# Performance work log

Hardware: AMD Instinct MI355X
Metric: run time of the kernel (lower is better)

## Reference

```python
import jax, jax.numpy as jnp
import numpy as np

N = 20000; DEG = 32; E = N * DEG; F = 142; D = 32; H = 4; HD = H * D; C = 2
_BN = np.float32(1.0 / np.sqrt(1.0 + 1e-5))  # eval-mode BatchNorm1d with running mean 0 / var 1


def _prelu(x, a):
    return jnp.where(x >= 0, x, a * x)


def _layernorm(x, g, b):
    m = x.mean(-1, keepdims=True)
    v = x.var(-1, keepdims=True)
    return (x - m) / jnp.sqrt(v + 1e-5) * g + b


def _conv(h, src, dst, Wq, bq, Wk, bk, Wv, bv, Ws, bs, Wg, bg, lng, lnb, a):
    # TransformerConv: u_dot_v attention (q from src, k from dst), edge softmax over
    # incoming edges of each dst node, u_mul_e + sum aggregation, gated skip, LN, PReLU.
    n = h.shape[0]
    q = (h @ Wq + bq).reshape(n, H, D)
    k = (h @ Wk + bk).reshape(n, H, D)
    v = (h @ Wv + bv).reshape(n, H, D)
    scores = jnp.einsum('ehd,ehd->eh', q[src], k[dst]) / np.float32(np.sqrt(D))  # [E,H]
    m = jax.ops.segment_max(scores, dst, num_segments=n)
    p = jnp.exp(scores - m[dst])
    s = jax.ops.segment_sum(p, dst, num_segments=n)
    sa = p / s[dst]                                                              # [E,H]
    agg = jax.ops.segment_sum(v[src] * sa[..., None], dst, num_segments=n)       # [N,H,D]
    agg = agg.reshape(n, HD)
    skip = h @ Ws + bs
    g = jax.nn.sigmoid(jnp.concatenate([skip, agg, skip - agg], -1) @ Wg + bg)
    rst = g * skip + (1.0 - g) * agg
    return _prelu(_layernorm(rst, lng, lnb), a)


def setup_inputs() -> dict:
    ks = jax.random.split(jax.random.key(0), 64)
    def nrm(i, shape, s=0.05):
        return (jax.random.normal(ks[i], shape) * s).astype(jnp.float32)
    inp = {}
    inp['features'] = jax.random.normal(ks[0], (N, F), jnp.float32)
    inp['label_emb'] = nrm(1, (C + 1, F)).at[C].set(0.0)  # padding_idx = n_classes
    inp['W1'] = nrm(2, (F, HD)); inp['b1'] = jnp.zeros(HD)
    inp['W2'] = nrm(3, (F, HD)); inp['b2'] = jnp.zeros(HD)
    inp['bn0_g'] = jnp.ones(HD); inp['bn0_b'] = jnp.zeros(HD)
    inp['a3'] = 0.25 * jnp.ones(1)
    inp['W3'] = nrm(4, (HD, F)); inp['b3'] = jnp.zeros(F)
    i = 5
    for l, fin in enumerate([F, HD]):
        inp[f'Wq{l}'] = nrm(i, (fin, HD)); i += 1
        inp[f'bq{l}'] = jnp.zeros(HD)
        inp[f'Wk{l}'] = nrm(i, (fin, HD)); i += 1
        inp[f'bk{l}'] = jnp.zeros(HD)
        inp[f'Wv{l}'] = nrm(i, (fin, HD)); i += 1
        inp[f'bv{l}'] = jnp.zeros(HD)
        inp[f'Ws{l}'] = nrm(i, (fin, HD)); i += 1
        inp[f'bs{l}'] = jnp.zeros(HD)
        inp[f'Wg{l}'] = nrm(i, (3 * HD, 1)); i += 1
        inp[f'bg{l}'] = jnp.zeros(1)
        inp[f'ln{l}_g'] = jnp.ones(HD)
        inp[f'ln{l}_b'] = jnp.zeros(HD)
    inp['a_conv'] = 0.25 * jnp.ones(1)  # single PReLU instance shared by both conv layers
    inp['W4'] = nrm(i, (HD, HD)); i += 1; inp['b4'] = jnp.zeros(HD)
    inp['bn1_g'] = jnp.ones(HD); inp['bn1_b'] = jnp.zeros(HD)
    inp['a5'] = 0.25 * jnp.ones(1)
    inp['W5'] = nrm(i, (HD, C)); i += 1; inp['b5'] = jnp.zeros(C)
    inp['labels'] = jax.random.randint(ks[40], (N,), 0, C + 1)
    inp['edge_src'] = jax.random.randint(ks[41], (E,), 0, N)
    inp['edge_dst'] = jnp.repeat(jnp.arange(N), DEG)  # every node has in-degree DEG
    return inp


def reference(features, label_emb, W1, b1, W2, b2, bn0_g, bn0_b, a3, W3, b3,
              Wq0, bq0, Wk0, bk0, Wv0, bv0, Ws0, bs0, Wg0, bg0, ln0_g, ln0_b,
              Wq1, bq1, Wk1, bk1, Wv1, bv1, Ws1, bs1, Wg1, bg1, ln1_g, ln1_b,
              a_conv, W4, b4, bn1_g, bn1_b, a5, W5, b5,
              labels, edge_src, edge_dst):
    le = label_emb[labels]                                   # [N,F]
    le = features @ W1 + b1 + le @ W2 + b2                   # [N,HD]
    le = _prelu(le * _BN * bn0_g + bn0_b, a3) @ W3 + b3      # BN -> PReLU -> Linear
    h = features + le
    h = _conv(h, edge_src, edge_dst, Wq0, bq0, Wk0, bk0, Wv0, bv0, Ws0, bs0, Wg0, bg0, ln0_g, ln0_b, a_conv)
    h = _conv(h, edge_src, edge_dst, Wq1, bq1, Wk1, bk1, Wv1, bv1, Ws1, bs1, Wg1, bg1, ln1_g, ln1_b, a_conv)
    x = h @ W4 + b4
    x = _prelu(x * _BN * bn1_g + bn1_b, a5)
    return x @ W5 + b5                                       # [N, n_classes]
```

## Files before the change

kernel.cpp:

```cpp
#include <hip/hip_runtime.h>
#include <math.h>

#define N_NODES 20000
#define DEG 32
#define F_IN 142
#define HD 128
#define NHEAD 4
#define DHEAD 32
#define N_CLS 2

#define BN_SCALE 0.9999950000374997f
#define INV_SQRT_D 0.17677669529663687f

typedef short v8s __attribute__((ext_vector_type(8)));
typedef float v4f __attribute__((ext_vector_type(4)));

__device__ __forceinline__ unsigned short f2bf(float f) {
    unsigned u = __float_as_uint(f);
    return (unsigned short)((u + 0x7fffu + ((u >> 16) & 1u)) >> 16);
}
__device__ __forceinline__ unsigned pack2bf(float a, float b) {
    return (unsigned)f2bf(a) | ((unsigned)f2bf(b) << 16);
}
__device__ __forceinline__ float bf2f(unsigned short s) {
    return __uint_as_float((unsigned)s << 16);
}
__device__ __forceinline__ float bflo(unsigned u) { return __uint_as_float(u << 16); }
__device__ __forceinline__ float bfhi(unsigned u) { return __uint_as_float(u & 0xffff0000u); }

__device__ __forceinline__ v8s pack8(float4 f0, float4 f1) {
    union { v8s s; unsigned u[4]; } x;
    x.u[0] = pack2bf(f0.x, f0.y);
    x.u[1] = pack2bf(f0.z, f0.w);
    x.u[2] = pack2bf(f1.x, f1.y);
    x.u[3] = pack2bf(f1.z, f1.w);
    return x.s;
}

__global__ void kE0(const float* __restrict__ lemb, const float* __restrict__ W2,
                    const float* __restrict__ b1, const float* __restrict__ b2,
                    float* __restrict__ E) {
    __shared__ float sl[F_IN];
    int l = blockIdx.x, c = threadIdx.x;
    for (int f = c; f < F_IN; f += HD) sl[f] = lemb[l * F_IN + f];
    __syncthreads();
    float acc = b1[c] + b2[c];
    for (int f = 0; f < F_IN; ++f) acc += sl[f] * W2[f * HD + c];
    E[l * HD + c] = acc;
}

template<int KC, int K>
__global__ void kSwiz4(const float* Wa, const float* Wb, const float* Wc,
                       const float* Wd, short* __restrict__ out) {
    const float* Wt[4] = {Wa, Wb, Wc, Wd};
    const float* W = Wt[blockIdx.y];
    const int tile = blockIdx.x;
    const int kc = tile % KC, nt = tile / KC;
    const int L = threadIdx.x;
    const int n = nt * 16 + (L & 15);
    const int kb = kc * 32 + (L >> 4) * 8;
    short v[8] __attribute__((aligned(16)));
    #pragma unroll
    for (int j = 0; j < 8; ++j) {
        int k = kb + j;
        v[j] = (k < K) ? (short)f2bf(W[(size_t)k * HD + n]) : (short)0;
    }
    short* dst = out + (size_t)blockIdx.y * (8 * KC * 64 * 8) + ((size_t)tile * 64 + L) * 8;
    *(uint4*)dst = *(const uint4*)v;
}

template<int KC, int K>
__global__ void kSwiz1(const float* __restrict__ W, short* __restrict__ out) {
    const int tile = blockIdx.x;
    const int kc = tile % KC, nt = tile / KC;
    const int L = threadIdx.x;
    const int n = nt * 16 + (L & 15);
    const int kb = kc * 32 + (L >> 4) * 8;
    short v[8] __attribute__((aligned(16)));
    #pragma unroll
    for (int j = 0; j < 8; ++j) {
        int k = kb + j;
        v[j] = (k < K) ? (short)f2bf(W[(size_t)k * HD + n]) : (short)0;
    }
    *(uint4*)(out + ((size_t)tile * 64 + L) * 8) = *(const uint4*)v;
}

__global__ void kSwizW3(const float* __restrict__ W3, short* __restrict__ out) {
    const int tile = blockIdx.x;
    const int kc = tile & 3, nt = tile >> 2;
    const int L = threadIdx.x;
    const int n = nt * 16 + (L & 15);
    const int kb = kc * 32 + (L >> 4) * 8;
    short v[8] __attribute__((aligned(16)));
    #pragma unroll
    for (int j = 0; j < 8; ++j)
        v[j] = (n < F_IN) ? (short)f2bf(W3[(size_t)(kb + j) * F_IN + n]) : (short)0;
    *(uint4*)(out + ((size_t)tile * 64 + L) * 8) = *(const uint4*)v;
}

__global__ __launch_bounds__(256) void kAB_m(const float* __restrict__ feat,
        const short* __restrict__ W1f, const short* __restrict__ W3f,
        const int* __restrict__ labels, const float* __restrict__ E,
        const float* __restrict__ bng, const float* __restrict__ bnb,
        const float* __restrict__ a3, const float* __restrict__ b3,
        float* __restrict__ h) {
    __shared__ float4 sAv[32 * 164 / 4];
    __shared__ uint4  sTv[32 * 136 / 8];
    __shared__ int sLab[32];
    float* sA = (float*)sAv;
    unsigned short* sT = (unsigned short*)sTv;
    const int tid = threadIdx.x;
    const int row0 = blockIdx.x * 32;
    for (int idx = tid; idx < 32 * F_IN; idx += 256) {
        int r = idx / F_IN, c = idx - r * F_IN;
        sA[r * 164 + c] = feat[(size_t)(row0 + r) * F_IN + c];
    }
    {   const int ZC = 160 - F_IN;
        for (int idx = tid; idx < 32 * ZC; idx += 256) {
            int r = idx / ZC, c = idx - r * ZC;
            sA[r * 164 + F_IN + c] = 0.f;
        }
    }
    if (tid < 32) sLab[tid] = labels[row0 + tid];
    __syncthreads();

    const int lane = tid & 63, w = tid >> 6;
    const int m = lane & 15, q = lane >> 4;
    const int nt0 = w * 2, nt1 = nt0 + 1;

    v4f acc00 = {0.f,0.f,0.f,0.f}, acc01 = acc00, acc10 = acc00, acc11 = acc00;
    #pragma unroll
    for (int kc = 0; kc < 5; ++kc) {
        const float* r0 = sA + m * 164 + kc * 32 + q * 8;
        const float* r1 = sA + (16 + m) * 164 + kc * 32 + q * 8;
        v8s a0 = pack8(*(const float4*)r0, *(const float4*)(r0 + 4));
        v8s a1 = pack8(*(const float4*)r1, *(const float4*)(r1 + 4));
        v8s b0 = *(const v8s*)(W1f + ((size_t)((nt0 * 5 + kc) * 64 + lane)) * 8);
        v8s b1 = *(const v8s*)(W1f + ((size_t)((nt1 * 5 + kc) * 64 + lane)) * 8);
        acc00 = __builtin_amdgcn_mfma_f32_16x16x32_bf16(a0, b0, acc00, 0, 0, 0);
        acc01 = __builtin_amdgcn_mfma_f32_16x16x32_bf16(a0, b1, acc01, 0, 0, 0);
        acc10 = __builtin_amdgcn_mfma_f32_16x16x32_bf16(a1, b0, acc10, 0, 0, 0);
        acc11 = __builtin_amdgcn_mfma_f32_16x16x32_bf16(a1, b1, acc11, 0, 0, 0);
    }
    const int c0 = w * 32 + m, c1 = c0 + 16;
    {
        const float g0 = bng[c0] * BN_SCALE, g1 = bng[c1] * BN_SCALE;
        const float bb0 = bnb[c0], bb1 = bnb[c1];
        const float al = a3[0];
        #pragma unroll
        for (int rt = 0; rt < 2; ++rt) {
            v4f A0 = rt ? acc10 : acc00;
            v4f A1 = rt ? acc11 : acc01;
            #pragma unroll
            for (int i = 0; i < 4; ++i) {
                const int r = rt * 16 + q * 4 + i;
                const int lab = sLab[r];
                float y0 = (A0[i] + E[lab * HD + c0]) * g0 + bb0;
                float y1 = (A1[i] + E[lab * HD + c1]) * g1 + bb1;
                y0 = (y0 >= 0.f) ? y0 : al * y0;
                y1 = (y1 >= 0.f) ? y1 : al * y1;
                sT[r * 136 + c0] = f2bf(y0);
                sT[r * 136 + c1] = f2bf(y1);
            }
        }
    }
    __syncthreads();

    v4f d00 = {0.f,0.f,0.f,0.f}, d01 = d00, d10 = d00, d11 = d00, e0 = d00, e1 = d00;
    #pragma unroll
    for (int kc = 0; kc < 4; ++kc) {
        v8s a0 = *(const v8s*)(sT + m * 136 + kc * 32 + q * 8);
        v8s a1 = *(const v8s*)(sT + (16 + m) * 136 + kc * 32 + q * 8);
        v8s b0 = *(const v8s*)(W3f + ((size_t)((nt0 * 4 + kc) * 64 + lane)) * 8);
        v8s b1 = *(const v8s*)(W3f + ((size_t)((nt1 * 4 + kc) * 64 + lane)) * 8);
        d00 = __builtin_amdgcn_mfma_f32_16x16x32_bf16(a0, b0, d00, 0, 0, 0);
        d01 = __builtin_amdgcn_mfma_f32_16x16x32_bf16(a0, b1, d01, 0, 0, 0);
        d10 = __builtin_amdgcn_mfma_f32_16x16x32_bf16(a1, b0, d10, 0, 0, 0);
        d11 = __builtin_amdgcn_mfma_f32_16x16x32_bf16(a1, b1, d11, 0, 0, 0);
        if (w == 3) {
            v8s b2 = *(const v8s*)(W3f + ((size_t)((8 * 4 + kc) * 64 + lane)) * 8);
            e0 = __builtin_amdgcn_mfma_f32_16x16x32_bf16(a0, b2, e0, 0, 0, 0);
            e1 = __builtin_amdgcn_mfma_f32_16x16x32_bf16(a1, b2, e1, 0, 0, 0);
        }
    }
    const float b30 = b3[c0], b31 = b3[c1];
    #pragma unroll
    for (int rt = 0; rt < 2; ++rt) {
        v4f D0 = rt ? d10 : d00;
        v4f D1 = rt ? d11 : d01;
        #pragma unroll
        for (int i = 0; i < 4; ++i) {
            const int r = row0 + rt * 16 + q * 4 + i;
            h[(size_t)r * F_IN + c0] = feat[(size_t)r * F_IN + c0] + D0[i] + b30;
            h[(size_t)r * F_IN + c1] = feat[(size_t)r * F_IN + c1] + D1[i] + b31;
        }
    }
    if (w == 3) {
        const int c2 = 128 + m;
        if (c2 < F_IN) {
            const float b32 = b3[c2];
            #pragma unroll
            for (int i = 0; i < 4; ++i) {
                const int ra = row0 + q * 4 + i;
                const int rb = ra + 16;
                h[(size_t)ra * F_IN + c2] = feat[(size_t)ra * F_IN + c2] + e0[i] + b32;
                h[(size_t)rb * F_IN + c2] = feat[(size_t)rb * F_IN + c2] + e1[i] + b32;
            }
        }
    }
}

template<int K, int LDSK, int KC>
__global__ __launch_bounds__(256) void kC4_mf(const float* __restrict__ A,
        const short* __restrict__ WfBase,
        const float* __restrict__ bq, const float* __restrict__ bk,
        const float* __restrict__ bv, const float* __restrict__ bs,
        unsigned short* __restrict__ qh, unsigned short* __restrict__ kh,
        unsigned short* __restrict__ vh, float* __restrict__ sOut) {
    __shared__ float4 sAv[32 * LDSK / 4];
    float* sA = (float*)sAv;
    const int tid = threadIdx.x;
    const int row0 = blockIdx.x * 32;
    for (int idx = tid; idx < 32 * K; idx += 256) {
        int r = idx / K, c = idx - r * K;
        sA[r * LDSK + c] = A[(size_t)(row0 + r) * K + c];
    }
    if (K < KC * 32) {
        const int ZC = KC * 32 - K;
        for (int idx = tid; idx < 32 * ZC; idx += 256) {
            int r = idx / ZC, c = idx - r * ZC;
            sA[r * LDSK + K + c] = 0.f;
        }
    }
    __syncthreads();

    const int lane = tid & 63, w = tid >> 6;
    const int m = lane & 15, q = lane >> 4;
    const int nt0 = w * 2, nt1 = nt0 + 1;

    v8s afr0[KC], afr1[KC];
    #pragma unroll
    for (int kc = 0; kc < KC; ++kc) {
        const float* r0 = sA + m * LDSK + kc * 32 + q * 8;
        const float* r1 = sA + (16 + m) * LDSK + kc * 32 + q * 8;
        afr0[kc] = pack8(*(const float4*)r0, *(const float4*)(r0 + 4));
        afr1[kc] = pack8(*(const float4*)r1, *(const float4*)(r1 + 4));
    }

    const int c0 = w * 32 + m, c1 = c0 + 16;
    #pragma unroll
    for (int mat = 0; mat < 4; ++mat) {
        const short* Wf = WfBase + (size_t)mat * (KC * 4096);
        const float* bias = (mat == 0) ? bq : (mat == 1) ? bk : (mat == 2) ? bv : bs;
        v4f acc00 = {0.f,0.f,0.f,0.f}, acc01 = acc00, acc10 = acc00, acc11 = acc00;
        #pragma unroll
        for (int kc = 0; kc < KC; ++kc) {
            v8s b0 = *(const v8s*)(Wf + ((size_t)((nt0 * KC + kc) * 64 + lane)) * 8);
            v8s b1 = *(const v8s*)(Wf + ((size_t)((nt1 * KC + kc) * 64 + lane)) * 8);
            acc00 = __builtin_amdgcn_mfma_f32_16x16x32_bf16(afr0[kc], b0, acc00, 0, 0, 0);
            acc01 = __builtin_amdgcn_mfma_f32_16x16x32_bf16(afr0[kc], b1, acc01, 0, 0, 0);
            acc10 = __builtin_amdgcn_mfma_f32_16x16x32_bf16(afr1[kc], b0, acc10, 0, 0, 0);
            acc11 = __builtin_amdgcn_mfma_f32_16x16x32_bf16(afr1[kc], b1, acc11, 0, 0, 0);
        }
        const float b0v = bias[c0], b1v = bias[c1];
        if (mat < 3) {
            unsigned short* outh = (mat == 0) ? qh : (mat == 1) ? kh : vh;
            unsigned short* outw = outh + ((size_t)w * N_NODES + row0) * DHEAD;
            #pragma unroll
            for (int rt = 0; rt < 2; ++rt) {
                v4f A0 = rt ? acc10 : acc00;
                v4f A1 = rt ? acc11 : acc01;
                #pragma unroll
                for (int i = 0; i < 4; ++i) {
                    const int r = rt * 16 + q * 4 + i;
                    outw[(size_t)r * DHEAD + m]      = f2bf(A0[i] + b0v);
                    outw[(size_t)r * DHEAD + 16 + m] = f2bf(A1[i] + b1v);
                }
            }
        } else {
            #pragma unroll
            for (int rt = 0; rt < 2; ++rt) {
                v4f A0 = rt ? acc10 : acc00;
                v4f A1 = rt ? acc11 : acc01;
                #pragma unroll
                for (int i = 0; i < 4; ++i) {
                    const int r = rt * 16 + q * 4 + i;
                    sOut[(size_t)(row0 + r) * HD + c0] = A0[i] + b0v;
                    sOut[(size_t)(row0 + r) * HD + c1] = A1[i] + b1v;
                }
            }
        }
    }
}

__global__ __launch_bounds__(256) void kD_h(const unsigned short* __restrict__ qh,
        const unsigned short* __restrict__ kh, const unsigned short* __restrict__ vh,
        const int* __restrict__ esrc, float* __restrict__ agg) {
    __shared__ float sk[8][DHEAD];
    __shared__ int ssrc[8][DEG];
    __shared__ float sa[8][DEG];
    const int h = blockIdx.y;
    const int n0 = blockIdx.x * 8;
    const int t = threadIdx.x;
    const int j = t >> 5, e = t & 31;

    ssrc[j][e] = esrc[n0 * DEG + t];
    if (t < 128) {
        unsigned u = *((const unsigned*)(kh + ((size_t)h * N_NODES + n0) * DHEAD) + t);
        float* skf = &sk[0][0];
        skf[2 * t]     = bflo(u);
        skf[2 * t + 1] = bfhi(u);
    }
    __syncthreads();

    const int src = ssrc[j][e];
    const uint4* qp = (const uint4*)(qh + ((size_t)h * N_NODES + src) * DHEAD);
    const float* kj = sk[j];
    float sc = 0.f;
    #pragma unroll
    for (int i = 0; i < 4; ++i) {
        uint4 u = qp[i];
        sc = fmaf(bflo(u.x), kj[i * 8 + 0], sc);
        sc = fmaf(bfhi(u.x), kj[i * 8 + 1], sc);
        sc = fmaf(bflo(u.y), kj[i * 8 + 2], sc);
        sc = fmaf(bfhi(u.y), kj[i * 8 + 3], sc);
        sc = fmaf(bflo(u.z), kj[i * 8 + 4], sc);
        sc = fmaf(bfhi(u.z), kj[i * 8 + 5], sc);
        sc = fmaf(bflo(u.w), kj[i * 8 + 6], sc);
        sc = fmaf(bfhi(u.w), kj[i * 8 + 7], sc);
    }
    sc *= INV_SQRT_D;
    float m = sc;
    #pragma unroll
    for (int off = 16; off > 0; off >>= 1)
        m = fmaxf(m, __shfl_xor(m, off, 32));
    float p = expf(sc - m);
    float ssum = p;
    #pragma unroll
    for (int off = 16; off > 0; off >>= 1)
        ssum += __shfl_xor(ssum, off, 32);
    sa[j][e] = p / ssum;
    __syncthreads();

    const int d = t & 31;
    const unsigned short* vbase = vh + (size_t)h * N_NODES * DHEAD + d;
    float acc = 0.f;
    #pragma unroll
    for (int e2 = 0; e2 < DEG; ++e2) {
        const int s2 = ssrc[j][e2];
        acc = fmaf(bf2f(vbase[(size_t)s2 * DHEAD]), sa[j][e2], acc);
    }
    agg[(size_t)(n0 + j) * HD + h * DHEAD + d] = acc;
}

__device__ __forceinline__ float blockSum128(float v, float* s2, int tid) {
    #pragma unroll
    for (int o = 32; o > 0; o >>= 1) v += __shfl_xor(v, o, 64);
    if ((tid & 63) == 0) s2[tid >> 6] = v;
    __syncthreads();
    float r = s2[0] + s2[1];
    __syncthreads();
    return r;
}

__global__ void kE(const float* __restrict__ skip, const float* __restrict__ agg,
                   const float* __restrict__ Wg, const float* __restrict__ bg,
                   const float* __restrict__ lng, const float* __restrict__ lnb,
                   const float* __restrict__ ac,
                   float* __restrict__ hout) {
    __shared__ float red[2];
    int n = blockIdx.x, c = threadIdx.x;
    float sk = skip[n * HD + c], ag = agg[n * HD + c];
    float part = sk * Wg[c] + ag * Wg[HD + c] + (sk - ag) * Wg[2 * HD + c];
    float z = blockSum128(part, red, c) + bg[0];
    float g = 1.f / (1.f + expf(-z));
    float r = g * sk + (1.f - g) * ag;
    float mean = blockSum128(r, red, c) * (1.f / HD);
    float dv = r - mean;
    float var = blockSum128(dv * dv, red, c) * (1.f / HD);
    float y = dv * rsqrtf(var + 1e-5f) * lng[c] + lnb[c];
    float a = ac[0];
    hout[n * HD + c] = (y >= 0.f) ? y : a * y;
}

__global__ __launch_bounds__(256) void kF_mf2(const float* __restrict__ A,
        const short* __restrict__ W4f, const float* __restrict__ b4,
        const float* __restrict__ bng, const float* __restrict__ bnb,
        const float* __restrict__ a5, const float* __restrict__ W5,
        const float* __restrict__ b5, float* __restrict__ out) {
    __shared__ float4 sAv[32 * 132 / 4];
    float* sA = (float*)sAv;
    const int tid = threadIdx.x;
    const int row0 = blockIdx.x * 32;
    for (int idx = tid; idx < 32 * HD; idx += 256) {
        int r = idx >> 7, c = idx & 127;
        sA[r * 132 + c] = A[(size_t)(row0 + r) * HD + c];
    }
    __syncthreads();
    const int lane = tid & 63, w = tid >> 6;
    const int m = lane & 15, q = lane >> 4;
    const int nt0 = w * 2, nt1 = nt0 + 1;
    v4f acc00 = {0.f,0.f,0.f,0.f}, acc01 = acc00, acc10 = acc00, acc11 = acc00;
    #pragma unroll
    for (int kc = 0; kc < 4; ++kc) {
        const float* r0 = sA + m * 132 + kc * 32 + q * 8;
        const float* r1 = sA + (16 + m) * 132 + kc * 32 + q * 8;
        v8s a0 = pack8(*(const float4*)r0, *(const float4*)(r0 + 4));
        v8s a1 = pack8(*(const float4*)r1, *(const float4*)(r1 + 4));
        v8s b0 = *(const v8s*)(W4f + ((size_t)((nt0 * 4 + kc) * 64 + lane)) * 8);
        v8s b1 = *(const v8s*)(W4f + ((size_t)((nt1 * 4 + kc) * 64 + lane)) * 8);
        acc00 = __builtin_amdgcn_mfma_f32_16x16x32_bf16(a0, b0, acc00, 0, 0, 0);
        acc01 = __builtin_amdgcn_mfma_f32_16x16x32_bf16(a0, b1, acc01, 0, 0, 0);
        acc10 = __builtin_amdgcn_mfma_f32_16x16x32_bf16(a1, b0, acc10, 0, 0, 0);
        acc11 = __builtin_amdgcn_mfma_f32_16x16x32_bf16(a1, b1, acc11, 0, 0, 0);
    }
    __syncthreads();
    const int c0 = w * 32 + m, c1 = c0 + 16;
    const float g0 = bng[c0] * BN_SCALE, g1 = bng[c1] * BN_SCALE;
    const float bb0 = bnb[c0], bb1 = bnb[c1];
    const float b40 = b4[c0], b41 = b4[c1];
    const float al = a5[0];
    #pragma unroll
    for (int rt = 0; rt < 2; ++rt) {
        v4f A0 = rt ? acc10 : acc00;
        v4f A1 = rt ? acc11 : acc01;
        #pragma unroll
        for (int i = 0; i < 4; ++i) {
            const int r = rt * 16 + q * 4 + i;
            float y0 = (A0[i] + b40) * g0 + bb0;
            float y1 = (A1[i] + b41) * g1 + bb1;
            y0 = (y0 >= 0.f) ? y0 : al * y0;
            y1 = (y1 >= 0.f) ? y1 : al * y1;
            sA[r * 132 + c0] = y0;
            sA[r * 132 + c1] = y1;
        }
    }
    __syncthreads();
    if (tid < 64) {
        const int r = tid >> 1, cls = tid & 1;
        const float* yr = sA + r * 132;
        float s = b5[cls];
        #pragma unroll 8
        for (int c = 0; c < HD; ++c)
            s = fmaf(yr[c], W5[c * 2 + cls], s);
        out[(size_t)(row0 + r) * N_CLS + cls] = s;
    }
}

extern "C" void kernel_launch(void* const* d_in, const int* in_sizes, int n_in,
                              void* d_out, int out_size, void* d_ws, size_t ws_size,
                              hipStream_t stream) {
    const float* feat  = (const float*)d_in[0];
    const float* lemb  = (const float*)d_in[1];
    const float* W1    = (const float*)d_in[2];
    const float* b1    = (const float*)d_in[3];
    const float* W2    = (const float*)d_in[4];
    const float* b2    = (const float*)d_in[5];
    const float* bn0g  = (const float*)d_in[6];
    const float* bn0b  = (const float*)d_in[7];
    const float* a3    = (const float*)d_in[8];
    const float* W3    = (const float*)d_in[9];
    const float* b3    = (const float*)d_in[10];
    const float* aconv = (const float*)d_in[35];
    const float* W4    = (const float*)d_in[36];
    const float* b4    = (const float*)d_in[37];
    const float* bn1g  = (const float*)d_in[38];
    const float* bn1b  = (const float*)d_in[39];
    const float* a5    = (const float*)d_in[40];
    const float* W5    = (const float*)d_in[41];
    const float* b5    = (const float*)d_in[42];
    const int*   labels = (const int*)d_in[43];
    const int*   esrc   = (const int*)d_in[44];

    char* ws = (char*)d_ws;
    float* bh  = (float*)ws;                       ws += sizeof(float) * N_NODES * F_IN;
    float* bs  = (float*)ws;                       ws += sizeof(float) * N_NODES * HD;
    float* bag = (float*)ws;                       ws += sizeof(float) * N_NODES * HD;
    float* bh2 = (float*)ws;                       ws += sizeof(float) * N_NODES * HD;
    unsigned short* bqh = (unsigned short*)ws;     ws += sizeof(short) * N_NODES * HD;
    unsigned short* bkh = (unsigned short*)ws;     ws += sizeof(short) * N_NODES * HD;
    unsigned short* bvh = (unsigned short*)ws;     ws += sizeof(short) * N_NODES * HD;
    short* Wf0 = (short*)ws;                       ws += sizeof(short) * 4 * 20480;
    short* Wf1 = (short*)ws;                       ws += sizeof(short) * 4 * 16384;
    short* W1f = (short*)ws;                       ws += sizeof(short) * 20480;
    short* W3f = (short*)ws;                       ws += sizeof(short) * 36 * 512;
    short* W4f = (short*)ws;                       ws += sizeof(short) * 16384;
    float* bE = bag;
    float* out = (float*)d_out;

    dim3 gT(N_NODES / 32);
    dim3 gD(N_NODES / 8, NHEAD);

    kE0<<<dim3(3), HD, 0, stream>>>(lemb, W2, b1, b2, bE);
    kSwiz4<5, F_IN><<<dim3(40, 4), 64, 0, stream>>>(
        (const float*)d_in[11], (const float*)d_in[13],
        (const float*)d_in[15], (const float*)d_in[17], Wf0);
    kSwiz4<4, HD><<<dim3(32, 4), 64, 0, stream>>>(
        (const float*)d_in[23], (const float*)d_in[25],
        (const float*)d_in[27], (const float*)d_in[29], Wf1);
    kSwiz1<5, F_IN><<<dim3(40), 64, 0, stream>>>(W1, W1f);
    kSwizW3<<<dim3(36), 64, 0, stream>>>(W3, W3f);
    kSwiz1<4, HD><<<dim3(32), 64, 0, stream>>>(W4, W4f);

    kAB_m<<<gT, 256, 0, stream>>>(feat, W1f, W3f, labels, bE, bn0g, bn0b, a3, b3, bh);

    kC4_mf<F_IN, 164, 5><<<gT, 256, 0, stream>>>(bh, Wf0,
        (const float*)d_in[12], (const float*)d_in[14],
        (const float*)d_in[16], (const float*)d_in[18],
        bqh, bkh, bvh, bs);
    kD_h<<<gD, 256, 0, stream>>>(bqh, bkh, bvh, esrc, bag);
    kE<<<dim3(N_NODES), HD, 0, stream>>>(bs, bag, (const float*)d_in[19], (const float*)d_in[20],
        (const float*)d_in[21], (const float*)d_in[22], aconv, bh2);

    kC4_mf<HD, 132, 4><<<gT, 256, 0, stream>>>(bh2, Wf1,
        (const float*)d_in[24], (const float*)d_in[26],
        (const float*)d_in[28], (const float*)d_in[30],
        bqh, bkh, bvh, bs);
    kD_h<<<gD, 256, 0, stream>>>(bqh, bkh, bvh, esrc, bag);
    kE<<<dim3(N_NODES), HD, 0, stream>>>(bs, bag, (const float*)d_in[31], (const float*)d_in[32],
        (const float*)d_in[33], (const float*)d_in[34], aconv, bh2);

    kF_mf2<<<gT, 256, 0, stream>>>(bh2, W4f, b4, bn1g, bn1b, a5, W5, b5, out);
}
```

Measured before the change: 328.5 us.

## Fuse attention aggregation with gated skip, LayerNorm and PReLU per node block

```diff
diff --git a/kernel.cpp b/kernel.cpp
--- a/kernel.cpp
+++ b/kernel.cpp
@@ -50,9 +50,9 @@
 }
 
 template<int KC, int K>
-__global__ void kSwiz4(const float* Wa, const float* Wb, const float* Wc,
-                       const float* Wd, short* __restrict__ out) {
-    const float* Wt[4] = {Wa, Wb, Wc, Wd};
+__global__ void kSwiz5(const float* Wa, const float* Wb, const float* Wc,
+                       const float* Wd, const float* We, short* __restrict__ out) {
+    const float* Wt[5] = {Wa, Wb, Wc, Wd, We};
     const float* W = Wt[blockIdx.y];
     const int tile = blockIdx.x;
     const int kc = tile % KC, nt = tile / KC;
@@ -67,22 +67,6 @@
     }
     short* dst = out + (size_t)blockIdx.y * (8 * KC * 64 * 8) + ((size_t)tile * 64 + L) * 8;
     *(uint4*)dst = *(const uint4*)v;
-}
-
-template<int KC, int K>
-__global__ void kSwiz1(const float* __restrict__ W, short* __restrict__ out) {
-    const int tile = blockIdx.x;
-    const int kc = tile % KC, nt = tile / KC;
-    const int L = threadIdx.x;
-    const int n = nt * 16 + (L & 15);
-    const int kb = kc * 32 + (L >> 4) * 8;
-    short v[8] __attribute__((aligned(16)));
-    #pragma unroll
-    for (int j = 0; j < 8; ++j) {
-        int k = kb + j;
-        v[j] = (k < K) ? (short)f2bf(W[(size_t)k * HD + n]) : (short)0;
-    }
-    *(uint4*)(out + ((size_t)tile * 64 + L) * 8) = *(const uint4*)v;
 }
 
 __global__ void kSwizW3(const float* __restrict__ W3, short* __restrict__ out) {
@@ -293,94 +277,115 @@
     }
 }
 
-__global__ __launch_bounds__(256) void kD_h(const unsigned short* __restrict__ qh,
+__global__ __launch_bounds__(256) void kDE_h(const unsigned short* __restrict__ qh,
         const unsigned short* __restrict__ kh, const unsigned short* __restrict__ vh,
-        const int* __restrict__ esrc, float* __restrict__ agg) {
+        const int* __restrict__ esrc, const float* __restrict__ skip,
+        const float* __restrict__ Wg, const float* __restrict__ bg,
+        const float* __restrict__ lng, const float* __restrict__ lnb,
+        const float* __restrict__ ac, float* __restrict__ hout) {
     __shared__ float sk[8][DHEAD];
     __shared__ int ssrc[8][DEG];
     __shared__ float sa[8][DEG];
-    const int h = blockIdx.y;
+    __shared__ float sAgg[8][HD];
     const int n0 = blockIdx.x * 8;
     const int t = threadIdx.x;
     const int j = t >> 5, e = t & 31;
 
     ssrc[j][e] = esrc[n0 * DEG + t];
-    if (t < 128) {
-        unsigned u = *((const unsigned*)(kh + ((size_t)h * N_NODES + n0) * DHEAD) + t);
-        float* skf = &sk[0][0];
-        skf[2 * t]     = bflo(u);
-        skf[2 * t + 1] = bfhi(u);
-    }
-    __syncthreads();
-
-    const int src = ssrc[j][e];
-    const uint4* qp = (const uint4*)(qh + ((size_t)h * N_NODES + src) * DHEAD);
-    const float* kj = sk[j];
-    float sc = 0.f;
-    #pragma unroll
-    for (int i = 0; i < 4; ++i) {
-        uint4 u = qp[i];
-        sc = fmaf(bflo(u.x), kj[i * 8 + 0], sc);
-        sc = fmaf(bfhi(u.x), kj[i * 8 + 1], sc);
-        sc = fmaf(bflo(u.y), kj[i * 8 + 2], sc);
-        sc = fmaf(bfhi(u.y), kj[i * 8 + 3], sc);
-        sc = fmaf(bflo(u.z), kj[i * 8 + 4], sc);
-        sc = fmaf(bfhi(u.z), kj[i * 8 + 5], sc);
-        sc = fmaf(bflo(u.w), kj[i * 8 + 6], sc);
-        sc = fmaf(bfhi(u.w), kj[i * 8 + 7], sc);
-    }
-    sc *= INV_SQRT_D;
-    float m = sc;
+
+    for (int h = 0; h < NHEAD; ++h) {
+        __syncthreads();
+        if (t < 128) {
+            unsigned u = *((const unsigned*)(kh + ((size_t)h * N_NODES + n0) * DHEAD) + t);
+            float* skf = &sk[0][0];
+            skf[2 * t]     = bflo(u);
+            skf[2 * t + 1] = bfhi(u);
+        }
+        __syncthreads();
+
+        const int src = ssrc[j][e];
+        const uint4* qp = (const uint4*)(qh + ((size_t)h * N_NODES + src) * DHEAD);
+        const float* kj = sk[j];
+        float sc = 0.f;
+        #pragma unroll
+        for (int i = 0; i < 4; ++i) {
+            uint4 u = qp[i];
+            sc = fmaf(bflo(u.x), kj[i * 8 + 0], sc);
+            sc = fmaf(bfhi(u.x), kj[i * 8 + 1], sc);
+            sc = fmaf(bflo(u.y), kj[i * 8 + 2], sc);
+            sc = fmaf(bfhi(u.y), kj[i * 8 + 3], sc);
+            sc = fmaf(bflo(u.z), kj[i * 8 + 4], sc);
+            sc = fmaf(bfhi(u.z), kj[i * 8 + 5], sc);
+            sc = fmaf(bflo(u.w), kj[i * 8 + 6], sc);
+            sc = fmaf(bfhi(u.w), kj[i * 8 + 7], sc);
+        }
+        sc *= INV_SQRT_D;
+        float mx = sc;
+        #pragma unroll
+        for (int off = 16; off > 0; off >>= 1)
+            mx = fmaxf(mx, __shfl_xor(mx, off, 32));
+        float p = expf(sc - mx);
+        float ssum = p;
+        #pragma unroll
+        for (int off = 16; off > 0; off >>= 1)
+            ssum += __shfl_xor(ssum, off, 32);
+        sa[j][e] = p / ssum;
+        __syncthreads();
+
+        const unsigned short* vbase = vh + (size_t)h * N_NODES * DHEAD + e;
+        float acc = 0.f;
+        #pragma unroll
+        for (int e2 = 0; e2 < DEG; ++e2) {
+            const int s2 = ssrc[j][e2];
+            acc = fmaf(bf2f(vbase[(size_t)s2 * DHEAD]), sa[j][e2], acc);
+        }
+        sAgg[j][h * DHEAD + e] = acc;
+    }
+    __syncthreads();
+
+    const int n = n0 + j;
+    float skv[4], agv[4];
+    float part = 0.f;
+    #pragma unroll
+    for (int k2 = 0; k2 < 4; ++k2) {
+        const int c = e + 32 * k2;
+        skv[k2] = skip[(size_t)n * HD + c];
+        agv[k2] = sAgg[j][c];
+        part += skv[k2] * Wg[c] + agv[k2] * Wg[HD + c] + (skv[k2] - agv[k2]) * Wg[2 * HD + c];
+    }
     #pragma unroll
     for (int off = 16; off > 0; off >>= 1)
-        m = fmaxf(m, __shfl_xor(m, off, 32));
-    float p = expf(sc - m);
-    float ssum = p;
+        part += __shfl_xor(part, off, 32);
+    const float z = part + bg[0];
+    const float g = 1.f / (1.f + expf(-z));
+    float rv[4], rsum = 0.f;
+    #pragma unroll
+    for (int k2 = 0; k2 < 4; ++k2) {
+        rv[k2] = g * skv[k2] + (1.f - g) * agv[k2];
+        rsum += rv[k2];
+    }
     #pragma unroll
     for (int off = 16; off > 0; off >>= 1)
-        ssum += __shfl_xor(ssum, off, 32);
-    sa[j][e] = p / ssum;
-    __syncthreads();
-
-    const int d = t & 31;
-    const unsigned short* vbase = vh + (size_t)h * N_NODES * DHEAD + d;
-    float acc = 0.f;
-    #pragma unroll
-    for (int e2 = 0; e2 < DEG; ++e2) {
-        const int s2 = ssrc[j][e2];
-        acc = fmaf(bf2f(vbase[(size_t)s2 * DHEAD]), sa[j][e2], acc);
-    }
-    agg[(size_t)(n0 + j) * HD + h * DHEAD + d] = acc;
-}
-
-__device__ __forceinline__ float blockSum128(float v, float* s2, int tid) {
-    #pragma unroll
-    for (int o = 32; o > 0; o >>= 1) v += __shfl_xor(v, o, 64);
-    if ((tid & 63) == 0) s2[tid >> 6] = v;
-    __syncthreads();
-    float r = s2[0] + s2[1];
-    __syncthreads();
-    return r;
-}
-
-__global__ void kE(const float* __restrict__ skip, const float* __restrict__ agg,
-                   const float* __restrict__ Wg, const float* __restrict__ bg,
-                   const float* __restrict__ lng, const float* __restrict__ lnb,
-                   const float* __restrict__ ac,
-                   float* __restrict__ hout) {
-    __shared__ float red[2];
-    int n = blockIdx.x, c = threadIdx.x;
-    float sk = skip[n * HD + c], ag = agg[n * HD + c];
-    float part = sk * Wg[c] + ag * Wg[HD + c] + (sk - ag) * Wg[2 * HD + c];
-    float z = blockSum128(part, red, c) + bg[0];
-    float g = 1.f / (1.f + expf(-z));
-    float r = g * sk + (1.f - g) * ag;
-    float mean = blockSum128(r, red, c) * (1.f / HD);
-    float dv = r - mean;
-    float var = blockSum128(dv * dv, red, c) * (1.f / HD);
-    float y = dv * rsqrtf(var + 1e-5f) * lng[c] + lnb[c];
-    float a = ac[0];
-    hout[n * HD + c] = (y >= 0.f) ? y : a * y;
+        rsum += __shfl_xor(rsum, off, 32);
+    const float mean = rsum * (1.f / HD);
+    float dv[4], vsum = 0.f;
+    #pragma unroll
+    for (int k2 = 0; k2 < 4; ++k2) {
+        dv[k2] = rv[k2] - mean;
+        vsum += dv[k2] * dv[k2];
+    }
+    #pragma unroll
+    for (int off = 16; off > 0; off >>= 1)
+        vsum += __shfl_xor(vsum, off, 32);
+    const float inv = rsqrtf(vsum * (1.f / HD) + 1e-5f);
+    const float al = ac[0];
+    #pragma unroll
+    for (int k2 = 0; k2 < 4; ++k2) {
+        const int c = e + 32 * k2;
+        float y = dv[k2] * inv * lng[c] + lnb[c];
+        y = (y >= 0.f) ? y : al * y;
+        hout[(size_t)n * HD + c] = y;
+    }
 }
 
 __global__ __launch_bounds__(256) void kF_mf2(const float* __restrict__ A,
@@ -475,50 +480,45 @@
     char* ws = (char*)d_ws;
     float* bh  = (float*)ws;                       ws += sizeof(float) * N_NODES * F_IN;
     float* bs  = (float*)ws;                       ws += sizeof(float) * N_NODES * HD;
-    float* bag = (float*)ws;                       ws += sizeof(float) * N_NODES * HD;
     float* bh2 = (float*)ws;                       ws += sizeof(float) * N_NODES * HD;
     unsigned short* bqh = (unsigned short*)ws;     ws += sizeof(short) * N_NODES * HD;
     unsigned short* bkh = (unsigned short*)ws;     ws += sizeof(short) * N_NODES * HD;
     unsigned short* bvh = (unsigned short*)ws;     ws += sizeof(short) * N_NODES * HD;
-    short* Wf0 = (short*)ws;                       ws += sizeof(short) * 4 * 20480;
-    short* Wf1 = (short*)ws;                       ws += sizeof(short) * 4 * 16384;
-    short* W1f = (short*)ws;                       ws += sizeof(short) * 20480;
+    short* Wf142 = (short*)ws;                     ws += sizeof(short) * 5 * 20480;
+    short* Wf128 = (short*)ws;                     ws += sizeof(short) * 5 * 16384;
     short* W3f = (short*)ws;                       ws += sizeof(short) * 36 * 512;
-    short* W4f = (short*)ws;                       ws += sizeof(short) * 16384;
-    float* bE = bag;
+    float* bE  = (float*)ws;                       ws += sizeof(float) * 3 * HD;
     float* out = (float*)d_out;
 
     dim3 gT(N_NODES / 32);
-    dim3 gD(N_NODES / 8, NHEAD);
+    dim3 gDE(N_NODES / 8);
 
     kE0<<<dim3(3), HD, 0, stream>>>(lemb, W2, b1, b2, bE);
-    kSwiz4<5, F_IN><<<dim3(40, 4), 64, 0, stream>>>(
+    kSwiz5<5, F_IN><<<dim3(40, 5), 64, 0, stream>>>(W1,
         (const float*)d_in[11], (const float*)d_in[13],
-        (const float*)d_in[15], (const float*)d_in[17], Wf0);
-    kSwiz4<4, HD><<<dim3(32, 4), 64, 0, stream>>>(
+        (const float*)d_in[15], (const float*)d_in[17], Wf142);
+    kSwiz5<4, HD><<<dim3(32, 5), 64, 0, stream>>>(
         (const float*)d_in[23], (const float*)d_in[25],
-        (const float*)d_in[27], (const float*)d_in[29], Wf1);
-    kSwiz1<5, F_IN><<<dim3(40), 64, 0, stream>>>(W1, W1f);
+        (const float*)d_in[27], (const float*)d_in[29], W4, Wf128);
     kSwizW3<<<dim3(36), 64, 0, stream>>>(W3, W3f);
-    kSwiz1<4, HD><<<dim3(32), 64, 0, stream>>>(W4, W4f);
-
-    kAB_m<<<gT, 256, 0, stream>>>(feat, W1f, W3f, labels, bE, bn0g, bn0b, a3, b3, bh);
-
-    kC4_mf<F_IN, 164, 5><<<gT, 256, 0, stream>>>(bh, Wf0,
+
+    kAB_m<<<gT, 256, 0, stream>>>(feat, Wf142, W3f, labels, bE, bn0g, bn0b, a3, b3, bh);
+
+    kC4_mf<F_IN, 164, 5><<<gT, 256, 0, stream>>>(bh, Wf142 + 20480,
         (const float*)d_in[12], (const float*)d_in[14],
         (const float*)d_in[16], (const float*)d_in[18],
         bqh, bkh, bvh, bs);
-    kD_h<<<gD, 256, 0, stream>>>(bqh, bkh, bvh, esrc, bag);
-    kE<<<dim3(N_NODES), HD, 0, stream>>>(bs, bag, (const float*)d_in[19], (const float*)d_in[20],
+    kDE_h<<<gDE, 256, 0, stream>>>(bqh, bkh, bvh, esrc, bs,
+        (const float*)d_in[19], (const float*)d_in[20],
         (const float*)d_in[21], (const float*)d_in[22], aconv, bh2);
 
-    kC4_mf<HD, 132, 4><<<gT, 256, 0, stream>>>(bh2, Wf1,
+    kC4_mf<HD, 132, 4><<<gT, 256, 0, stream>>>(bh2, Wf128,
         (const float*)d_in[24], (const float*)d_in[26],
         (const float*)d_in[28], (const float*)d_in[30],
         bqh, bkh, bvh, bs);
-    kD_h<<<gD, 256, 0, stream>>>(bqh, bkh, bvh, esrc, bag);
-    kE<<<dim3(N_NODES), HD, 0, stream>>>(bs, bag, (const float*)d_in[31], (const float*)d_in[32],
+    kDE_h<<<gDE, 256, 0, stream>>>(bqh, bkh, bvh, esrc, bs,
+        (const float*)d_in[31], (const float*)d_in[32],
         (const float*)d_in[33], (const float*)d_in[34], aconv, bh2);
 
-    kF_mf2<<<gT, 256, 0, stream>>>(bh2, W4f, b4, bn1g, bn1b, a5, W5, b5, out);
-}
+    kF_mf2<<<gT, 256, 0, stream>>>(bh2, Wf128 + 4 * 16384, b4, bn1g, bn1b, a5, W5, b5, out);
+}
```

Measured after the change: 331.4 us. Within noise of the previous version (+0.9%).
